# Performance work log

Hardware: AMD Instinct MI355X
Metric: run time of the kernel (lower is better)

## Reference

```python
import jax, jax.numpy as jnp
import numpy as np

B, S, H = 4, 2048, 1024
E = 8
INTER = 2816  # round(4.0*1024*2/3)=2731 -> next multiple of 256


def setup_inputs() -> dict:
    key = jax.random.key(0)
    k1, k2, k3, k4 = jax.random.split(key, 4)
    x = jax.random.normal(k1, (B, S, H), dtype=jnp.float32)
    gate_w = jax.random.normal(k2, (E, H), dtype=jnp.float32) * 0.02
    w_gate_up = jax.random.normal(k3, (E, H, 2 * INTER), dtype=jnp.float32) * 0.02
    w_down = jax.random.normal(k4, (E, INTER, H), dtype=jnp.float32) * 0.02
    return {"x": x, "gate_w": gate_w, "w_gate_up": w_gate_up, "w_down": w_down, "top_k": 2}


def _moe(x, gate_w, w_gate_up, w_down, top_k):
    Bx, Sx, Hx = x.shape
    Ex = gate_w.shape[0]
    T = Bx * Sx
    # Router
    logits = jnp.einsum('bsh,eh->bse', x, gate_w)
    probs = jax.nn.softmax(logits.astype(jnp.float32), axis=-1)  # [B,S,E] fp32
    topk_vals, topk_idx = jax.lax.top_k(probs, top_k)             # [B,S,K]
    topk_w = topk_vals / jnp.clip(topk_vals.sum(-1, keepdims=True), 1e-8)
    importance = probs.mean((0, 1))                               # [E]
    onehot = jax.nn.one_hot(topk_idx, Ex, dtype=probs.dtype)      # [B,S,K,E]
    sel_mask = onehot.sum(-2)                                     # [B,S,E] 0/1 (topk unique)
    load = sel_mask.sum((0, 1)) / (T * top_k)
    aux_loss = (Ex * (importance * load)).sum()
    # Dense combine weights per token/expert (scatter_add equivalent)
    W_full = (onehot * topk_w[..., None]).sum(-2)                 # [B,S,E]
    x_flat = x.reshape(T, Hx)
    W_flat = W_full.reshape(T, Ex).astype(x.dtype)
    out = jnp.zeros_like(x_flat)
    for e in range(Ex):  # fixed small expert loop
        gu = x_flat @ w_gate_up[e]                                # [T, 2I]
        g, u = jnp.split(gu, 2, axis=-1)
        y = (jax.nn.silu(g) * u) @ w_down[e]                      # [T, H]
        out = out + y * W_flat[:, e:e + 1]
    return out.reshape(Bx, Sx, Hx), aux_loss


def reference(x, gate_w, w_gate_up, w_down, top_k):
    return _moe(x, gate_w, w_gate_up, w_down, int(top_k))
```

## Files before the change

### kernel.cpp

```cpp
#include <hip/hip_runtime.h>

#define E_ 8
#define H_ 1024
#define I_ 2816
#define GU_ 5632
#define T_ 8192
#define NBR_ 2048

typedef __attribute__((ext_vector_type(8))) __bf16 bf16x8;
typedef __attribute__((ext_vector_type(4))) float f32x4;
typedef __attribute__((ext_vector_type(8))) unsigned short u16x8;
typedef __attribute__((ext_vector_type(4))) unsigned short u16x4;
typedef unsigned short u16;

__device__ __forceinline__ float bf2f(u16 u) {
  union { unsigned int i; float f; } v; v.i = ((unsigned int)u) << 16; return v.f;
}
__device__ __forceinline__ u16 f2bf(float f) {
  union { float f; unsigned int i; } v; v.f = f;
  unsigned int r = v.i + 0x7fffu + ((v.i >> 16) & 1u);
  return (u16)(r >> 16);
}
__device__ __forceinline__ void gld16(const void* g, void* l) {
  __builtin_amdgcn_global_load_lds((const __attribute__((address_space(1))) void*)g,
                                   (__attribute__((address_space(3))) void*)l, 16, 0, 0);
}

#define BAR() __builtin_amdgcn_s_barrier()
#define VMC(n) asm volatile("s_waitcnt vmcnt(" #n ")" ::: "memory")

__global__ __launch_bounds__(256) void k_router(
    const float* __restrict__ x, const float* __restrict__ gw,
    float* __restrict__ part_imp, int* __restrict__ part_cnt,
    int* __restrict__ tok_e, float* __restrict__ tok_w,
    u16* __restrict__ xb)
{
  __shared__ float s_imp[8];
  __shared__ int s_cnt[8];
  if (threadIdx.x < 8) { s_imp[threadIdx.x] = 0.f; s_cnt[threadIdx.x] = 0; }
  __syncthreads();

  const int t = blockIdx.x * 4 + (threadIdx.x >> 6);
  const int lane = threadIdx.x & 63;
  const float* xr = x + (size_t)t * H_;
  const f32x4* xp = (const f32x4*)(xr + lane * 16);
  f32x4 v0 = xp[0], v1 = xp[1], v2 = xp[2], v3 = xp[3];
  float xv[16];
#pragma unroll
  for (int b = 0; b < 4; ++b) { xv[b] = v0[b]; xv[4+b] = v1[b]; xv[8+b] = v2[b]; xv[12+b] = v3[b]; }
  u16x8 o0, o1;
#pragma unroll
  for (int j = 0; j < 8; ++j) { o0[j] = f2bf(xv[j]); o1[j] = f2bf(xv[8 + j]); }
  *(u16x8*)(xb + (size_t)t * H_ + lane * 16) = o0;
  *(u16x8*)(xb + (size_t)t * H_ + lane * 16 + 8) = o1;

  float lg[8];
#pragma unroll
  for (int e = 0; e < 8; ++e) {
    const f32x4* gp = (const f32x4*)(gw + e * H_ + lane * 16);
    float s = 0.f;
#pragma unroll
    for (int a = 0; a < 4; ++a) {
      f32x4 g4 = gp[a];
#pragma unroll
      for (int b = 0; b < 4; ++b) s += xv[a * 4 + b] * g4[b];
    }
    lg[e] = s;
  }
#pragma unroll
  for (int e = 0; e < 8; ++e)
#pragma unroll
    for (int off = 32; off; off >>= 1) lg[e] += __shfl_xor(lg[e], off);

  float m = lg[0];
#pragma unroll
  for (int e = 1; e < 8; ++e) m = fmaxf(m, lg[e]);
  float p[8], sum = 0.f;
#pragma unroll
  for (int e = 0; e < 8; ++e) { p[e] = __expf(lg[e] - m); sum += p[e]; }
  float inv = 1.f / sum;
#pragma unroll
  for (int e = 0; e < 8; ++e) p[e] *= inv;
  int e0 = 0;
#pragma unroll
  for (int e = 1; e < 8; ++e) if (p[e] > p[e0]) e0 = e;
  int e1 = (e0 == 0) ? 1 : 0;
#pragma unroll
  for (int e = 0; e < 8; ++e) if (e != e0 && p[e] > p[e1]) e1 = e;
  float d = 1.f / (p[e0] + p[e1]);
  if (lane == 0) {
#pragma unroll
    for (int e = 0; e < 8; ++e) atomicAdd(&s_imp[e], p[e]);
    atomicAdd(&s_cnt[e0], 1);
    atomicAdd(&s_cnt[e1], 1);
    tok_e[2 * t] = e0; tok_e[2 * t + 1] = e1;
    tok_w[2 * t] = p[e0] * d; tok_w[2 * t + 1] = p[e1] * d;
  }
  __syncthreads();
  if (threadIdx.x < 8) {
    part_imp[blockIdx.x * 8 + threadIdx.x] = s_imp[threadIdx.x];
    part_cnt[blockIdx.x * 8 + threadIdx.x] = s_cnt[threadIdx.x];
  }
}

__global__ __launch_bounds__(512) void k_reduce_scan(
    const float* __restrict__ part_imp, const int* __restrict__ part_cnt,
    int* __restrict__ counts, int* __restrict__ offsets, float* __restrict__ out)
{
  const int w = threadIdx.x >> 6, lane = threadIdx.x & 63;
  float si = 0.f; int sc = 0;
  for (int b = lane; b < NBR_; b += 64) { si += part_imp[b * 8 + w]; sc += part_cnt[b * 8 + w]; }
#pragma unroll
  for (int off = 32; off; off >>= 1) { si += __shfl_xor(si, off); sc += __shfl_xor(sc, off); }
  __shared__ float fimp[8];
  __shared__ int fcnt[8];
  if (lane == 0) { fimp[w] = si; fcnt[w] = sc; }
  __syncthreads();
  if (threadIdx.x == 0) {
    int off = 0; float aux = 0.f;
#pragma unroll
    for (int e = 0; e < 8; ++e) {
      counts[e] = fcnt[e]; offsets[e] = off; off += fcnt[e];
      aux += fimp[e] * (float)fcnt[e];
    }
    out[(size_t)T_ * H_] = 8.f * aux / ((float)T_ * (float)(2 * T_));
  }
}

__global__ __launch_bounds__(256) void k_scatter(
    const int* __restrict__ tok_e, const float* __restrict__ tok_w,
    const int* __restrict__ offsets, int* __restrict__ cursors,
    int* __restrict__ rows, float* __restrict__ wslot, int* __restrict__ t2s)
{
  __shared__ int lcnt[8], lbase[8];
  if (threadIdx.x < 8) lcnt[threadIdx.x] = 0;
  __syncthreads();
  const int t = blockIdx.x * 256 + threadIdx.x;
  const int e0 = tok_e[2 * t], e1 = tok_e[2 * t + 1];
  const int p0 = atomicAdd(&lcnt[e0], 1);
  const int p1 = atomicAdd(&lcnt[e1], 1);
  __syncthreads();
  if (threadIdx.x < 8) lbase[threadIdx.x] = atomicAdd(&cursors[threadIdx.x], lcnt[threadIdx.x]);
  __syncthreads();
  const int s0 = offsets[e0] + lbase[e0] + p0;
  const int s1 = offsets[e1] + lbase[e1] + p1;
  rows[s0] = t; wslot[s0] = tok_w[2 * t];     t2s[2 * t] = s0;
  rows[s1] = t; wslot[s1] = tok_w[2 * t + 1]; t2s[2 * t + 1] = s1;
}

__global__ __launch_bounds__(256) void k_transpose(
    const float* __restrict__ src, u16* __restrict__ dst, int R, int C)
{
  __shared__ float tile[64][68];
  const int z = blockIdx.z;
  const int c0 = blockIdx.x * 64, r0 = blockIdx.y * 64;
  const float* s = src + (size_t)z * R * C;
  u16* d = dst + (size_t)z * R * C;
  const int tx = threadIdx.x & 15, ty = threadIdx.x >> 4;
#pragma unroll
  for (int i = 0; i < 4; ++i) {
    f32x4 v = *(const f32x4*)(s + (size_t)(r0 + ty + i * 16) * C + c0 + tx * 4);
    *(f32x4*)(&tile[ty + i * 16][tx * 4]) = v;
  }
  __syncthreads();
  const int c = threadIdx.x >> 2, rq = threadIdx.x & 3;
#pragma unroll
  for (int j = 0; j < 4; ++j) {
    u16x4 w;
#pragma unroll
    for (int m = 0; m < 4; ++m) w[m] = f2bf(tile[rq * 16 + j * 4 + m][c]);
    *(u16x4*)(&d[(size_t)(c0 + c) * R + r0 + rq * 16 + j * 4]) = w;
  }
}

__global__ __launch_bounds__(256, 2) void k_gemm1(
    const u16* __restrict__ xb, const u16* __restrict__ wgu_t,
    const int* __restrict__ counts, const int* __restrict__ offsets,
    const int* __restrict__ rows, const float* __restrict__ wslot,
    u16* __restrict__ act)
{
  extern __shared__ char sh[];
  const int bid = blockIdx.x;
  const int l = (bid & 7) * 2816 + (bid >> 3);
  const int e = l / 2816;
  const int rm = l - e * 2816;
  const int xt = rm & 63, yt = rm >> 6;
  const int cnt = counts[e];
  const int m0 = xt * 128;
  if (m0 >= cnt) return;
  const int seg = offsets[e];
  const int segLast = seg + cnt - 1;
  const int n0 = yt * 64;

  const int tid = threadIdx.x;
  const int wid = tid >> 6, lane = tid & 63, l15 = lane & 15;
  const int srow = tid >> 3;
  const int scol = (((tid & 7) ^ (srow & 7)) * 8);

  const u16* wge = wgu_t + (size_t)e * GU_ * H_;

  const u16* aPtr[4];
#pragma unroll
  for (int i = 0; i < 4; ++i) {
    int slot = seg + m0 + i * 32 + srow;
    aPtr[i] = xb + (size_t)rows[slot > segLast ? segLast : slot] * H_ + scol;
  }
  const u16* bPtr[4];
  bPtr[0] = wge + (size_t)(n0 + srow) * H_ + scol;
  bPtr[1] = wge + (size_t)(n0 + 32 + srow) * H_ + scol;
  bPtr[2] = wge + (size_t)(I_ + n0 + srow) * H_ + scol;
  bPtr[3] = wge + (size_t)(I_ + n0 + 32 + srow) * H_ + scol;

  const int wm = (wid >> 1) * 64;
  const int wn = (wid & 1) * 32;

  f32x4 accg[4][2], accu[4][2];
#pragma unroll
  for (int i = 0; i < 4; ++i)
#pragma unroll
    for (int j = 0; j < 2; ++j) { accg[i][j] = (f32x4){0.f,0.f,0.f,0.f}; accu[i][j] = (f32x4){0.f,0.f,0.f,0.f}; }

#define G1_A(b, kt) { const int k0 = (kt) * 64; char* d = sh + (b) * 32768 + tid * 16;          \
    gld16(aPtr[0] + k0, d); gld16(aPtr[1] + k0, d + 4096);                                      \
    gld16(aPtr[2] + k0, d + 8192); gld16(aPtr[3] + k0, d + 12288); }
#define G1_B(b, kt) { const int k0 = (kt) * 64; char* d = sh + (b) * 32768 + 16384 + tid * 16;  \
    gld16(bPtr[0] + k0, d); gld16(bPtr[1] + k0, d + 4096);                                      \
    gld16(bPtr[2] + k0, d + 8192); gld16(bPtr[3] + k0, d + 12288); }

  const int NT = H_ / 64;
  G1_A(0, 0) G1_B(0, 0) G1_A(1, 1)
  VMC(4);
  BAR();

  int cur = 0;
  for (int t = 0; t < NT; ++t) {
    G1_B(cur ^ 1, (t + 1 < NT) ? t + 1 : NT - 1);
    const u16* As = (const u16*)(sh + cur * 32768);
    const u16* Bs = As + 8192;
#pragma unroll
    for (int ks = 0; ks < 2; ++ks) {
      const int koff = (ks * 32 + (lane >> 4) * 8) ^ ((lane & 7) * 8);
      bf16x8 a[4], bg[2], bu[2];
#pragma unroll
      for (int mf = 0; mf < 4; ++mf)
        a[mf] = *(const bf16x8*)(As + (wm + mf * 16 + l15) * 64 + koff);
#pragma unroll
      for (int nf = 0; nf < 2; ++nf) {
        bg[nf] = *(const bf16x8*)(Bs + (wn + nf * 16 + l15) * 64 + koff);
        bu[nf] = *(const bf16x8*)(Bs + (64 + wn + nf * 16 + l15) * 64 + koff);
      }
      __builtin_amdgcn_s_setprio(1);
#pragma unroll
      for (int mf = 0; mf < 4; ++mf)
#pragma unroll
        for (int nf = 0; nf < 2; ++nf) {
          accg[mf][nf] = __builtin_amdgcn_mfma_f32_16x16x32_bf16(a[mf], bg[nf], accg[mf][nf], 0, 0, 0);
          accu[mf][nf] = __builtin_amdgcn_mfma_f32_16x16x32_bf16(a[mf], bu[nf], accu[mf][nf], 0, 0, 0);
        }
      __builtin_amdgcn_s_setprio(0);
    }
    asm volatile("" ::: "memory");
    BAR();
    G1_A(cur, (t + 2 < NT) ? t + 2 : NT - 1);
    VMC(4);
    BAR();
    cur ^= 1;
  }
  VMC(0);
#undef G1_A
#undef G1_B

#pragma unroll
  for (int mf = 0; mf < 4; ++mf)
#pragma unroll
    for (int reg = 0; reg < 4; ++reg) {
      const int r = wm + mf * 16 + (lane >> 4) * 4 + reg;
      if (m0 + r >= cnt) continue;
      const int slot = seg + m0 + r;
      const float w = wslot[slot];
#pragma unroll
      for (int nf = 0; nf < 2; ++nf) {
        float g = accg[mf][nf][reg];
        float u = accu[mf][nf][reg];
        float sv = (g / (1.f + __expf(-g))) * u * w;
        act[(size_t)slot * I_ + n0 + wn + nf * 16 + l15] = f2bf(sv);
      }
    }
}

__global__ __launch_bounds__(256, 2) void k_gemm2(
    const u16* __restrict__ act, const u16* __restrict__ wd_t,
    const int* __restrict__ counts, const int* __restrict__ offsets,
    u16* __restrict__ y)
{
  extern __shared__ char sh[];
  const int bid = blockIdx.x;
  const int l = (bid & 7) * 512 + (bid >> 3);
  const int e = l >> 9;
  const int rm = l & 511;
  const int xt = rm & 63, yt = rm >> 6;
  const int cnt = counts[e];
  const int m0 = xt * 128;
  if (m0 >= cnt) return;
  const int seg = offsets[e];
  const int segLast = seg + cnt - 1;
  const int n0 = yt * 128;

  const int tid = threadIdx.x;
  const int wid = tid >> 6, lane = tid & 63, l15 = lane & 15;
  const int srow = tid >> 3;
  const int scol = (((tid & 7) ^ (srow & 7)) * 8);

  const u16* wde = wd_t + (size_t)e * H_ * I_;

  const u16* aPtr[4];
#pragma unroll
  for (int i = 0; i < 4; ++i) {
    int slot = seg + m0 + i * 32 + srow;
    aPtr[i] = act + (size_t)(slot > segLast ? segLast : slot) * I_ + scol;
  }
  const u16* bPtr[4];
#pragma unroll
  for (int i = 0; i < 4; ++i)
    bPtr[i] = wde + (size_t)(n0 + i * 32 + srow) * I_ + scol;

  const int wm = (wid >> 1) * 64;
  const int wn = (wid & 1) * 64;

  f32x4 acc[4][4];
#pragma unroll
  for (int i = 0; i < 4; ++i)
#pragma unroll
    for (int j = 0; j < 4; ++j) acc[i][j] = (f32x4){0.f,0.f,0.f,0.f};

#define G2_A(b, kt) { const int k0 = (kt) * 64; char* d = sh + (b) * 32768 + tid * 16;          \
    gld16(aPtr[0] + k0, d); gld16(aPtr[1] + k0, d + 4096);                                      \
    gld16(aPtr[2] + k0, d + 8192); gld16(aPtr[3] + k0, d + 12288); }
#define G2_B(b, kt) { const int k0 = (kt) * 64; char* d = sh + (b) * 32768 + 16384 + tid * 16;  \
    gld16(bPtr[0] + k0, d); gld16(bPtr[1] + k0, d + 4096);                                      \
    gld16(bPtr[2] + k0, d + 8192); gld16(bPtr[3] + k0, d + 12288); }

  const int NT = I_ / 64;
  G2_A(0, 0) G2_B(0, 0) G2_A(1, 1)
  VMC(4);
  BAR();

  int cur = 0;
  for (int t = 0; t < NT; ++t) {
    G2_B(cur ^ 1, (t + 1 < NT) ? t + 1 : NT - 1);
    const u16* As = (const u16*)(sh + cur * 32768);
    const u16* Bs = As + 8192;
#pragma unroll
    for (int ks = 0; ks < 2; ++ks) {
      const int koff = (ks * 32 + (lane >> 4) * 8) ^ ((lane & 7) * 8);
      bf16x8 a[4], b[4];
#pragma unroll
      for (int mf = 0; mf < 4; ++mf)
        a[mf] = *(const bf16x8*)(As + (wm + mf * 16 + l15) * 64 + koff);
#pragma unroll
      for (int nf = 0; nf < 4; ++nf)
        b[nf] = *(const bf16x8*)(Bs + (wn + nf * 16 + l15) * 64 + koff);
      __builtin_amdgcn_s_setprio(1);
#pragma unroll
      for (int mf = 0; mf < 4; ++mf)
#pragma unroll
        for (int nf = 0; nf < 4; ++nf)
          acc[mf][nf] = __builtin_amdgcn_mfma_f32_16x16x32_bf16(a[mf], b[nf], acc[mf][nf], 0, 0, 0);
      __builtin_amdgcn_s_setprio(0);
    }
    asm volatile("" ::: "memory");
    BAR();
    G2_A(cur, (t + 2 < NT) ? t + 2 : NT - 1);
    VMC(4);
    BAR();
    cur ^= 1;
  }
  VMC(0);
#undef G2_A
#undef G2_B

#pragma unroll
  for (int mf = 0; mf < 4; ++mf)
#pragma unroll
    for (int reg = 0; reg < 4; ++reg) {
      const int r = wm + mf * 16 + (lane >> 4) * 4 + reg;
      if (m0 + r >= cnt) continue;
      const int slot = seg + m0 + r;
#pragma unroll
      for (int nf = 0; nf < 4; ++nf)
        y[(size_t)slot * H_ + n0 + wn + nf * 16 + l15] = f2bf(acc[mf][nf][reg]);
    }
}

__global__ __launch_bounds__(256) void k_combine(
    const u16* __restrict__ y, const int* __restrict__ t2s, float* __restrict__ out)
{
  const size_t idx = ((size_t)blockIdx.x * 256 + threadIdx.x) * 8;
  const int t = (int)(idx >> 10);
  const int h = (int)(idx & 1023);
  const int s0 = t2s[2 * t], s1 = t2s[2 * t + 1];
  u16x8 a = *(const u16x8*)(y + (size_t)s0 * H_ + h);
  u16x8 b = *(const u16x8*)(y + (size_t)s1 * H_ + h);
  f32x4 o0, o1;
#pragma unroll
  for (int j = 0; j < 4; ++j) o0[j] = bf2f(a[j]) + bf2f(b[j]);
#pragma unroll
  for (int j = 0; j < 4; ++j) o1[j] = bf2f(a[4 + j]) + bf2f(b[4 + j]);
  *(f32x4*)(out + idx) = o0;
  *(f32x4*)(out + idx + 4) = o1;
}

extern "C" void kernel_launch(void* const* d_in, const int* in_sizes, int n_in,
                              void* d_out, int out_size, void* d_ws, size_t ws_size,
                              hipStream_t stream)
{
  const float* x   = (const float*)d_in[0];
  const float* gw  = (const float*)d_in[1];
  const float* wgu = (const float*)d_in[2];
  const float* wd  = (const float*)d_in[3];
  float* out = (float*)d_out;
  char* ws = (char*)d_ws;

  const size_t off_wgu_t = 0;
  const size_t off_wd_t  = off_wgu_t + (size_t)E_ * GU_ * H_ * 2;
  const size_t off_xb    = off_wd_t  + (size_t)E_ * H_ * I_ * 2;
  const size_t off_act   = off_xb    + (size_t)T_ * H_ * 2;
  const size_t off_ctrl  = off_act   + (size_t)2 * T_ * I_ * 2;
  const size_t need = off_ctrl + 128 + 5 * 65536;
  if (ws_size < need) return;

  u16* wgu_t = (u16*)(ws + off_wgu_t);
  u16* wd_t  = (u16*)(ws + off_wd_t);
  u16* xb    = (u16*)(ws + off_xb);
  u16* act   = (u16*)(ws + off_act);
  u16* y     = (u16*)(ws + off_wgu_t);
  float* part_imp = (float*)(ws + off_act);
  int*   part_cnt = (int*)(ws + off_act + (size_t)NBR_ * 8 * 4);
  char* ctrl = ws + off_ctrl;
  int*   counts  = (int*)(ctrl + 0);
  int*   cursors = (int*)(ctrl + 32);
  int*   offsets = (int*)(ctrl + 64);
  int*   tok_e   = (int*)(ctrl + 128);
  float* tok_w   = (float*)(ctrl + 128 + 1 * 65536);
  int*   rows    = (int*)(ctrl + 128 + 2 * 65536);
  float* wslot   = (float*)(ctrl + 128 + 3 * 65536);
  int*   t2s     = (int*)(ctrl + 128 + 4 * 65536);

  static bool attr_done = false;
  if (!attr_done) {
    hipFuncSetAttribute((const void*)k_gemm1, hipFuncAttributeMaxDynamicSharedMemorySize, 65536);
    hipFuncSetAttribute((const void*)k_gemm2, hipFuncAttributeMaxDynamicSharedMemorySize, 65536);
    attr_done = true;
  }

  hipMemsetAsync(ctrl, 0, 96, stream);
  hipLaunchKernelGGL(k_transpose, dim3(GU_ / 64, H_ / 64, E_), dim3(256), 0, stream, wgu, wgu_t, H_, GU_);
  hipLaunchKernelGGL(k_transpose, dim3(H_ / 64, I_ / 64, E_), dim3(256), 0, stream, wd, wd_t, I_, H_);
  hipLaunchKernelGGL(k_router, dim3(NBR_), dim3(256), 0, stream, x, gw, part_imp, part_cnt, tok_e, tok_w, xb);
  hipLaunchKernelGGL(k_reduce_scan, dim3(1), dim3(512), 0, stream, part_imp, part_cnt, counts, offsets, out);
  hipLaunchKernelGGL(k_scatter, dim3(T_ / 256), dim3(256), 0, stream, tok_e, tok_w, offsets, cursors, rows, wslot, t2s);
  hipLaunchKernelGGL(k_gemm1, dim3((I_ / 64) * 64 * E_), dim3(256), 65536, stream, xb, wgu_t, counts, offsets, rows, wslot, act);
  hipLaunchKernelGGL(k_gemm2, dim3((H_ / 128) * 64 * E_), dim3(256), 65536, stream, act, wd_t, counts, offsets, y);
  hipLaunchKernelGGL(k_combine, dim3((T_ * H_) / (256 * 8)), dim3(256), 0, stream, y, t2s, out);
}
```

Before: 545.8 us.

## Replace double-buffered LDS pipeline with single-buffer loop and higher occupancy

Both grouped GEMM kernels drop the two-stage double-buffered global-to-LDS prefetch and use a single 32KB static LDS buffer, loading each K tile and then synchronizing before compute. Launch bounds rise from 2 to 4 blocks per CU, relying on occupancy instead of software pipelining to hide memory latency. The dynamic shared-memory attribute setup is removed. This halves LDS per block but exposes load latency within each block and adds a full barrier wait on every iteration.

```diff
diff --git a/kernel.cpp b/kernel.cpp
--- a/kernel.cpp
+++ b/kernel.cpp
@@ -26,9 +26,6 @@
                                    (__attribute__((address_space(3))) void*)l, 16, 0, 0);
 }
 
-#define BAR() __builtin_amdgcn_s_barrier()
-#define VMC(n) asm volatile("s_waitcnt vmcnt(" #n ")" ::: "memory")
-
 __global__ __launch_bounds__(256) void k_router(
     const float* __restrict__ x, const float* __restrict__ gw,
     float* __restrict__ part_imp, int* __restrict__ part_cnt,
@@ -173,13 +170,13 @@
   }
 }
 
-__global__ __launch_bounds__(256, 2) void k_gemm1(
+__global__ __launch_bounds__(256, 4) void k_gemm1(
     const u16* __restrict__ xb, const u16* __restrict__ wgu_t,
     const int* __restrict__ counts, const int* __restrict__ offsets,
     const int* __restrict__ rows, const float* __restrict__ wslot,
     u16* __restrict__ act)
 {
-  extern __shared__ char sh[];
+  __shared__ alignas(16) char sh[32768];
   const int bid = blockIdx.x;
   const int l = (bid & 7) * 2816 + (bid >> 3);
   const int e = l / 2816;
@@ -220,22 +217,20 @@
 #pragma unroll
     for (int j = 0; j < 2; ++j) { accg[i][j] = (f32x4){0.f,0.f,0.f,0.f}; accu[i][j] = (f32x4){0.f,0.f,0.f,0.f}; }
 
-#define G1_A(b, kt) { const int k0 = (kt) * 64; char* d = sh + (b) * 32768 + tid * 16;          \
-    gld16(aPtr[0] + k0, d); gld16(aPtr[1] + k0, d + 4096);                                      \
-    gld16(aPtr[2] + k0, d + 8192); gld16(aPtr[3] + k0, d + 12288); }
-#define G1_B(b, kt) { const int k0 = (kt) * 64; char* d = sh + (b) * 32768 + 16384 + tid * 16;  \
-    gld16(bPtr[0] + k0, d); gld16(bPtr[1] + k0, d + 4096);                                      \
-    gld16(bPtr[2] + k0, d + 8192); gld16(bPtr[3] + k0, d + 12288); }
-
   const int NT = H_ / 64;
-  G1_A(0, 0) G1_B(0, 0) G1_A(1, 1)
-  VMC(4);
-  BAR();
-
-  int cur = 0;
   for (int t = 0; t < NT; ++t) {
-    G1_B(cur ^ 1, (t + 1 < NT) ? t + 1 : NT - 1);
-    const u16* As = (const u16*)(sh + cur * 32768);
+    {
+      char* dA = sh + tid * 16;
+      gld16(aPtr[0], dA); gld16(aPtr[1], dA + 4096);
+      gld16(aPtr[2], dA + 8192); gld16(aPtr[3], dA + 12288);
+      char* dB = sh + 16384 + tid * 16;
+      gld16(bPtr[0], dB); gld16(bPtr[1], dB + 4096);
+      gld16(bPtr[2], dB + 8192); gld16(bPtr[3], dB + 12288);
+#pragma unroll
+      for (int i = 0; i < 4; ++i) { aPtr[i] += 64; bPtr[i] += 64; }
+    }
+    __syncthreads();
+    const u16* As = (const u16*)sh;
     const u16* Bs = As + 8192;
 #pragma unroll
     for (int ks = 0; ks < 2; ++ks) {
@@ -259,16 +254,8 @@
         }
       __builtin_amdgcn_s_setprio(0);
     }
-    asm volatile("" ::: "memory");
-    BAR();
-    G1_A(cur, (t + 2 < NT) ? t + 2 : NT - 1);
-    VMC(4);
-    BAR();
-    cur ^= 1;
-  }
-  VMC(0);
-#undef G1_A
-#undef G1_B
+    __syncthreads();
+  }
 
 #pragma unroll
   for (int mf = 0; mf < 4; ++mf)
@@ -288,12 +275,12 @@
     }
 }
 
-__global__ __launch_bounds__(256, 2) void k_gemm2(
+__global__ __launch_bounds__(256, 4) void k_gemm2(
     const u16* __restrict__ act, const u16* __restrict__ wd_t,
     const int* __restrict__ counts, const int* __restrict__ offsets,
     u16* __restrict__ y)
 {
-  extern __shared__ char sh[];
+  __shared__ alignas(16) char sh[32768];
   const int bid = blockIdx.x;
   const int l = (bid & 7) * 512 + (bid >> 3);
   const int e = l >> 9;
@@ -333,22 +320,20 @@
 #pragma unroll
     for (int j = 0; j < 4; ++j) acc[i][j] = (f32x4){0.f,0.f,0.f,0.f};
 
-#define G2_A(b, kt) { const int k0 = (kt) * 64; char* d = sh + (b) * 32768 + tid * 16;          \
-    gld16(aPtr[0] + k0, d); gld16(aPtr[1] + k0, d + 4096);                                      \
-    gld16(aPtr[2] + k0, d + 8192); gld16(aPtr[3] + k0, d + 12288); }
-#define G2_B(b, kt) { const int k0 = (kt) * 64; char* d = sh + (b) * 32768 + 16384 + tid * 16;  \
-    gld16(bPtr[0] + k0, d); gld16(bPtr[1] + k0, d + 4096);                                      \
-    gld16(bPtr[2] + k0, d + 8192); gld16(bPtr[3] + k0, d + 12288); }
-
   const int NT = I_ / 64;
-  G2_A(0, 0) G2_B(0, 0) G2_A(1, 1)
-  VMC(4);
-  BAR();
-
-  int cur = 0;
   for (int t = 0; t < NT; ++t) {
-    G2_B(cur ^ 1, (t + 1 < NT) ? t + 1 : NT - 1);
-    const u16* As = (const u16*)(sh + cur * 32768);
+    {
+      char* dA = sh + tid * 16;
+      gld16(aPtr[0], dA); gld16(aPtr[1], dA + 4096);
+      gld16(aPtr[2], dA + 8192); gld16(aPtr[3], dA + 12288);
+      char* dB = sh + 16384 + tid * 16;
+      gld16(bPtr[0], dB); gld16(bPtr[1], dB + 4096);
+      gld16(bPtr[2], dB + 8192); gld16(bPtr[3], dB + 12288);
+#pragma unroll
+      for (int i = 0; i < 4; ++i) { aPtr[i] += 64; bPtr[i] += 64; }
+    }
+    __syncthreads();
+    const u16* As = (const u16*)sh;
     const u16* Bs = As + 8192;
 #pragma unroll
     for (int ks = 0; ks < 2; ++ks) {
@@ -368,16 +353,8 @@
           acc[mf][nf] = __builtin_amdgcn_mfma_f32_16x16x32_bf16(a[mf], b[nf], acc[mf][nf], 0, 0, 0);
       __builtin_amdgcn_s_setprio(0);
     }
-    asm volatile("" ::: "memory");
-    BAR();
-    G2_A(cur, (t + 2 < NT) ? t + 2 : NT - 1);
-    VMC(4);
-    BAR();
-    cur ^= 1;
-  }
-  VMC(0);
-#undef G2_A
-#undef G2_B
+    __syncthreads();
+  }
 
 #pragma unroll
   for (int mf = 0; mf < 4; ++mf)
@@ -446,20 +423,13 @@
   float* wslot   = (float*)(ctrl + 128 + 3 * 65536);
   int*   t2s     = (int*)(ctrl + 128 + 4 * 65536);
 
-  static bool attr_done = false;
-  if (!attr_done) {
-    hipFuncSetAttribute((const void*)k_gemm1, hipFuncAttributeMaxDynamicSharedMemorySize, 65536);
-    hipFuncSetAttribute((const void*)k_gemm2, hipFuncAttributeMaxDynamicSharedMemorySize, 65536);
-    attr_done = true;
-  }
-
   hipMemsetAsync(ctrl, 0, 96, stream);
   hipLaunchKernelGGL(k_transpose, dim3(GU_ / 64, H_ / 64, E_), dim3(256), 0, stream, wgu, wgu_t, H_, GU_);
   hipLaunchKernelGGL(k_transpose, dim3(H_ / 64, I_ / 64, E_), dim3(256), 0, stream, wd, wd_t, I_, H_);
   hipLaunchKernelGGL(k_router, dim3(NBR_), dim3(256), 0, stream, x, gw, part_imp, part_cnt, tok_e, tok_w, xb);
   hipLaunchKernelGGL(k_reduce_scan, dim3(1), dim3(512), 0, stream, part_imp, part_cnt, counts, offsets, out);
   hipLaunchKernelGGL(k_scatter, dim3(T_ / 256), dim3(256), 0, stream, tok_e, tok_w, offsets, cursors, rows, wslot, t2s);
-  hipLaunchKernelGGL(k_gemm1, dim3((I_ / 64) * 64 * E_), dim3(256), 65536, stream, xb, wgu_t, counts, offsets, rows, wslot, act);
-  hipLaunchKernelGGL(k_gemm2, dim3((H_ / 128) * 64 * E_), dim3(256), 65536, stream, act, wd_t, counts, offsets, y);
+  hipLaunchKernelGGL(k_gemm1, dim3((I_ / 64) * 64 * E_), dim3(256), 0, stream, xb, wgu_t, counts, offsets, rows, wslot, act);
+  hipLaunchKernelGGL(k_gemm2, dim3((H_ / 128) * 64 * E_), dim3(256), 0, stream, act, wd_t, counts, offsets, y);
   hipLaunchKernelGGL(k_combine, dim3((T_ * H_) / (256 * 8)), dim3(256), 0, stream, y, t2s, out);
 }
```

After: 548.5 us. About the same (+0.5%).

## Enlarge expert GEMM tiles to 256-row, 8-wave blocks with interleaved ping-pong schedule

Applied to the files above, without the earlier changes.

Both grouped expert GEMMs move from 128-row tiles with 4 waves to 256-row by 128-column tiles with 8 waves (512 threads) and 128 KB of double-buffered LDS. Each K-step is split into four quarter-phases in which LDS reads, async global-to-LDS loads of the next tiles and MFMA bursts are interleaved under explicit barriers, lgkmcnt waits and scheduling barriers. The aim is to raise arithmetic intensity per loaded byte and overlap memory traffic with matrix math. In exchange, LDS use caps residency at one block per CU, accumulator register pressure doubles, and the extra barriers may cost more than they save.

```diff
diff --git a/kernel.cpp b/kernel.cpp
--- a/kernel.cpp
+++ b/kernel.cpp
@@ -27,6 +27,8 @@
 }
 
 #define BAR() __builtin_amdgcn_s_barrier()
+#define SB0() __builtin_amdgcn_sched_barrier(0)
+#define LGKM0() asm volatile("s_waitcnt lgkmcnt(0)" ::: "memory")
 #define VMC(n) asm volatile("s_waitcnt vmcnt(" #n ")" ::: "memory")
 
 __global__ __launch_bounds__(256) void k_router(
@@ -173,7 +175,7 @@
   }
 }
 
-__global__ __launch_bounds__(256, 2) void k_gemm1(
+__global__ __launch_bounds__(512, 2) void k_gemm1(
     const u16* __restrict__ xb, const u16* __restrict__ wgu_t,
     const int* __restrict__ counts, const int* __restrict__ offsets,
     const int* __restrict__ rows, const float* __restrict__ wslot,
@@ -181,126 +183,12 @@
 {
   extern __shared__ char sh[];
   const int bid = blockIdx.x;
-  const int l = (bid & 7) * 2816 + (bid >> 3);
-  const int e = l / 2816;
-  const int rm = l - e * 2816;
+  const int l = (bid & 7) * 1408 + (bid >> 3);
+  const int e = l / 1408;
+  const int rm = l - e * 1408;
   const int xt = rm & 63, yt = rm >> 6;
   const int cnt = counts[e];
-  const int m0 = xt * 128;
-  if (m0 >= cnt) return;
-  const int seg = offsets[e];
-  const int segLast = seg + cnt - 1;
-  const int n0 = yt * 64;
-
-  const int tid = threadIdx.x;
-  const int wid = tid >> 6, lane = tid & 63, l15 = lane & 15;
-  const int srow = tid >> 3;
-  const int scol = (((tid & 7) ^ (srow & 7)) * 8);
-
-  const u16* wge = wgu_t + (size_t)e * GU_ * H_;
-
-  const u16* aPtr[4];
-#pragma unroll
-  for (int i = 0; i < 4; ++i) {
-    int slot = seg + m0 + i * 32 + srow;
-    aPtr[i] = xb + (size_t)rows[slot > segLast ? segLast : slot] * H_ + scol;
-  }
-  const u16* bPtr[4];
-  bPtr[0] = wge + (size_t)(n0 + srow) * H_ + scol;
-  bPtr[1] = wge + (size_t)(n0 + 32 + srow) * H_ + scol;
-  bPtr[2] = wge + (size_t)(I_ + n0 + srow) * H_ + scol;
-  bPtr[3] = wge + (size_t)(I_ + n0 + 32 + srow) * H_ + scol;
-
-  const int wm = (wid >> 1) * 64;
-  const int wn = (wid & 1) * 32;
-
-  f32x4 accg[4][2], accu[4][2];
-#pragma unroll
-  for (int i = 0; i < 4; ++i)
-#pragma unroll
-    for (int j = 0; j < 2; ++j) { accg[i][j] = (f32x4){0.f,0.f,0.f,0.f}; accu[i][j] = (f32x4){0.f,0.f,0.f,0.f}; }
-
-#define G1_A(b, kt) { const int k0 = (kt) * 64; char* d = sh + (b) * 32768 + tid * 16;          \
-    gld16(aPtr[0] + k0, d); gld16(aPtr[1] + k0, d + 4096);                                      \
-    gld16(aPtr[2] + k0, d + 8192); gld16(aPtr[3] + k0, d + 12288); }
-#define G1_B(b, kt) { const int k0 = (kt) * 64; char* d = sh + (b) * 32768 + 16384 + tid * 16;  \
-    gld16(bPtr[0] + k0, d); gld16(bPtr[1] + k0, d + 4096);                                      \
-    gld16(bPtr[2] + k0, d + 8192); gld16(bPtr[3] + k0, d + 12288); }
-
-  const int NT = H_ / 64;
-  G1_A(0, 0) G1_B(0, 0) G1_A(1, 1)
-  VMC(4);
-  BAR();
-
-  int cur = 0;
-  for (int t = 0; t < NT; ++t) {
-    G1_B(cur ^ 1, (t + 1 < NT) ? t + 1 : NT - 1);
-    const u16* As = (const u16*)(sh + cur * 32768);
-    const u16* Bs = As + 8192;
-#pragma unroll
-    for (int ks = 0; ks < 2; ++ks) {
-      const int koff = (ks * 32 + (lane >> 4) * 8) ^ ((lane & 7) * 8);
-      bf16x8 a[4], bg[2], bu[2];
-#pragma unroll
-      for (int mf = 0; mf < 4; ++mf)
-        a[mf] = *(const bf16x8*)(As + (wm + mf * 16 + l15) * 64 + koff);
-#pragma unroll
-      for (int nf = 0; nf < 2; ++nf) {
-        bg[nf] = *(const bf16x8*)(Bs + (wn + nf * 16 + l15) * 64 + koff);
-        bu[nf] = *(const bf16x8*)(Bs + (64 + wn + nf * 16 + l15) * 64 + koff);
-      }
-      __builtin_amdgcn_s_setprio(1);
-#pragma unroll
-      for (int mf = 0; mf < 4; ++mf)
-#pragma unroll
-        for (int nf = 0; nf < 2; ++nf) {
-          accg[mf][nf] = __builtin_amdgcn_mfma_f32_16x16x32_bf16(a[mf], bg[nf], accg[mf][nf], 0, 0, 0);
-          accu[mf][nf] = __builtin_amdgcn_mfma_f32_16x16x32_bf16(a[mf], bu[nf], accu[mf][nf], 0, 0, 0);
-        }
-      __builtin_amdgcn_s_setprio(0);
-    }
-    asm volatile("" ::: "memory");
-    BAR();
-    G1_A(cur, (t + 2 < NT) ? t + 2 : NT - 1);
-    VMC(4);
-    BAR();
-    cur ^= 1;
-  }
-  VMC(0);
-#undef G1_A
-#undef G1_B
-
-#pragma unroll
-  for (int mf = 0; mf < 4; ++mf)
-#pragma unroll
-    for (int reg = 0; reg < 4; ++reg) {
-      const int r = wm + mf * 16 + (lane >> 4) * 4 + reg;
-      if (m0 + r >= cnt) continue;
-      const int slot = seg + m0 + r;
-      const float w = wslot[slot];
-#pragma unroll
-      for (int nf = 0; nf < 2; ++nf) {
-        float g = accg[mf][nf][reg];
-        float u = accu[mf][nf][reg];
-        float sv = (g / (1.f + __expf(-g))) * u * w;
-        act[(size_t)slot * I_ + n0 + wn + nf * 16 + l15] = f2bf(sv);
-      }
-    }
-}
-
-__global__ __launch_bounds__(256, 2) void k_gemm2(
-    const u16* __restrict__ act, const u16* __restrict__ wd_t,
-    const int* __restrict__ counts, const int* __restrict__ offsets,
-    u16* __restrict__ y)
-{
-  extern __shared__ char sh[];
-  const int bid = blockIdx.x;
-  const int l = (bid & 7) * 512 + (bid >> 3);
-  const int e = l >> 9;
-  const int rm = l & 511;
-  const int xt = rm & 63, yt = rm >> 6;
-  const int cnt = counts[e];
-  const int m0 = xt * 128;
+  const int m0 = xt * 256;
   if (m0 >= cnt) return;
   const int seg = offsets[e];
   const int segLast = seg + cnt - 1;
@@ -308,87 +196,234 @@
 
   const int tid = threadIdx.x;
   const int wid = tid >> 6, lane = tid & 63, l15 = lane & 15;
+  const int wr = wid >> 2, wc = wid & 3;
   const int srow = tid >> 3;
   const int scol = (((tid & 7) ^ (srow & 7)) * 8);
 
-  const u16* wde = wd_t + (size_t)e * H_ * I_;
-
-  const u16* aPtr[4];
-#pragma unroll
-  for (int i = 0; i < 4; ++i) {
-    int slot = seg + m0 + i * 32 + srow;
-    aPtr[i] = act + (size_t)(slot > segLast ? segLast : slot) * I_ + scol;
-  }
-  const u16* bPtr[4];
-#pragma unroll
-  for (int i = 0; i < 4; ++i)
-    bPtr[i] = wde + (size_t)(n0 + i * 32 + srow) * I_ + scol;
-
-  const int wm = (wid >> 1) * 64;
-  const int wn = (wid & 1) * 64;
-
-  f32x4 acc[4][4];
-#pragma unroll
-  for (int i = 0; i < 4; ++i)
-#pragma unroll
-    for (int j = 0; j < 4; ++j) acc[i][j] = (f32x4){0.f,0.f,0.f,0.f};
-
-#define G2_A(b, kt) { const int k0 = (kt) * 64; char* d = sh + (b) * 32768 + tid * 16;          \
-    gld16(aPtr[0] + k0, d); gld16(aPtr[1] + k0, d + 4096);                                      \
-    gld16(aPtr[2] + k0, d + 8192); gld16(aPtr[3] + k0, d + 12288); }
-#define G2_B(b, kt) { const int k0 = (kt) * 64; char* d = sh + (b) * 32768 + 16384 + tid * 16;  \
-    gld16(bPtr[0] + k0, d); gld16(bPtr[1] + k0, d + 4096);                                      \
-    gld16(bPtr[2] + k0, d + 8192); gld16(bPtr[3] + k0, d + 12288); }
-
-  const int NT = I_ / 64;
-  G2_A(0, 0) G2_B(0, 0) G2_A(1, 1)
-  VMC(4);
-  BAR();
+  const u16* wge = wgu_t + (size_t)e * GU_ * H_;
+
+  const u16* aP[4];
+#pragma unroll
+  for (int g = 0; g < 4; ++g) {
+    int slot = seg + m0 + g * 64 + srow;
+    aP[g] = xb + (size_t)rows[slot > segLast ? segLast : slot] * H_ + scol;
+  }
+  const u16* bP[4];
+#pragma unroll
+  for (int j = 0; j < 4; ++j) {
+    int i = j & 1, half = j >> 1;
+    int br = (i * 2 + (srow >> 5)) * 64 + half * 32 + (srow & 31);
+    int g16 = br >> 4, sub = br & 15;
+    int grow = ((g16 & 1) ? I_ : 0) + n0 + (g16 >> 1) * 16 + sub;
+    bP[j] = wge + (size_t)grow * H_ + scol;
+  }
+
+  int koffs[2];
+#pragma unroll
+  for (int ks = 0; ks < 2; ++ks)
+    koffs[ks] = ((ks * 32 + (lane >> 4) * 8) ^ ((lane & 7) * 8)) * 2;
+
+  f32x4 accg[8][2], accu[8][2];
+#pragma unroll
+  for (int i = 0; i < 8; ++i)
+#pragma unroll
+    for (int j = 0; j < 2; ++j) { accg[i][j] = (f32x4){0.f,0.f,0.f,0.f}; accu[i][j] = (f32x4){0.f,0.f,0.f,0.f}; }
+
+#define ST_Aa(b, kt) { char* d = sh + (b)*65536 + tid*16;          gld16(aP[0]+(kt)*64, d); gld16(aP[2]+(kt)*64, d+8192); }
+#define ST_Ab(b, kt) { char* d = sh + (b)*65536 + 16384 + tid*16;  gld16(aP[1]+(kt)*64, d); gld16(aP[3]+(kt)*64, d+8192); }
+#define ST_Ba(b, kt) { char* d = sh + (b)*65536 + 32768 + tid*16;  gld16(bP[0]+(kt)*64, d); gld16(bP[1]+(kt)*64, d+8192); }
+#define ST_Bb(b, kt) { char* d = sh + (b)*65536 + 49152 + tid*16;  gld16(bP[2]+(kt)*64, d); gld16(bP[3]+(kt)*64, d+8192); }
+#define RD_A(MH) _Pragma("unroll") for (int ks=0;ks<2;++ks) _Pragma("unroll") for (int mf=0;mf<4;++mf) \
+  af[ks][mf] = *(const bf16x8*)(bufp + (MH)*16384 + (wr*64 + mf*16 + l15)*128 + koffs[ks]);
+#define RD_B(NH, DST) _Pragma("unroll") for (int ks=0;ks<2;++ks) _Pragma("unroll") for (int nfp=0;nfp<2;++nfp) \
+  DST[ks][nfp] = *(const bf16x8*)(bufp + 32768 + (NH)*16384 + (wc*32 + nfp*16 + l15)*128 + koffs[ks]);
+#define MM_G1(MB, CG, BSRC) \
+  __builtin_amdgcn_s_setprio(1); \
+  _Pragma("unroll") for (int ks=0;ks<2;++ks) _Pragma("unroll") for (int mf=0;mf<4;++mf) { \
+    accg[(MB)+mf][CG] = __builtin_amdgcn_mfma_f32_16x16x32_bf16(af[ks][mf], BSRC[ks][0], accg[(MB)+mf][CG],0,0,0); \
+    accu[(MB)+mf][CG] = __builtin_amdgcn_mfma_f32_16x16x32_bf16(af[ks][mf], BSRC[ks][1], accu[(MB)+mf][CG],0,0,0); \
+  } \
+  __builtin_amdgcn_s_setprio(0);
+
+  const int NT = H_ / 64;
+  ST_Aa(0,0) ST_Ba(0,0) ST_Ab(0,0) ST_Bb(0,0)
+  ST_Aa(1,1) ST_Ba(1,1) ST_Ab(1,1)
+  VMC(6); BAR();
 
   int cur = 0;
   for (int t = 0; t < NT; ++t) {
-    G2_B(cur ^ 1, (t + 1 < NT) ? t + 1 : NT - 1);
-    const u16* As = (const u16*)(sh + cur * 32768);
-    const u16* Bs = As + 8192;
-#pragma unroll
-    for (int ks = 0; ks < 2; ++ks) {
-      const int koff = (ks * 32 + (lane >> 4) * 8) ^ ((lane & 7) * 8);
-      bf16x8 a[4], b[4];
-#pragma unroll
-      for (int mf = 0; mf < 4; ++mf)
-        a[mf] = *(const bf16x8*)(As + (wm + mf * 16 + l15) * 64 + koff);
-#pragma unroll
-      for (int nf = 0; nf < 4; ++nf)
-        b[nf] = *(const bf16x8*)(Bs + (wn + nf * 16 + l15) * 64 + koff);
-      __builtin_amdgcn_s_setprio(1);
-#pragma unroll
-      for (int mf = 0; mf < 4; ++mf)
-#pragma unroll
-        for (int nf = 0; nf < 4; ++nf)
-          acc[mf][nf] = __builtin_amdgcn_mfma_f32_16x16x32_bf16(a[mf], b[nf], acc[mf][nf], 0, 0, 0);
-      __builtin_amdgcn_s_setprio(0);
-    }
-    asm volatile("" ::: "memory");
-    BAR();
-    G2_A(cur, (t + 2 < NT) ? t + 2 : NT - 1);
-    VMC(4);
+    const int nx1 = (t + 1 < NT) ? t + 1 : NT - 1;
+    const int nx2 = (t + 2 < NT) ? t + 2 : NT - 1;
+    const char* bufp = sh + cur * 65536;
+    bf16x8 af[2][4], bLo[2][2], bHi[2][2];
+    RD_A(0) RD_B(0, bLo)
+    ST_Bb(cur ^ 1, nx1)
+    BAR(); LGKM0(); SB0();
+    MM_G1(0, 0, bLo)
+    BAR();
+    RD_B(1, bHi)
+    ST_Aa(cur, nx2)
+    BAR(); LGKM0(); SB0();
+    MM_G1(0, 1, bHi)
+    BAR();
+    RD_A(1)
+    ST_Ba(cur, nx2)
+    BAR(); LGKM0(); SB0();
+    MM_G1(4, 0, bLo)
+    BAR();
+    ST_Ab(cur, nx2)
+    BAR();
+    MM_G1(4, 1, bHi)
+    VMC(6);
     BAR();
     cur ^= 1;
   }
   VMC(0);
-#undef G2_A
-#undef G2_B
-
-#pragma unroll
-  for (int mf = 0; mf < 4; ++mf)
+#undef ST_Aa
+#undef ST_Ab
+#undef ST_Ba
+#undef ST_Bb
+#undef RD_A
+#undef RD_B
+#undef MM_G1
+
+#pragma unroll
+  for (int mf = 0; mf < 8; ++mf)
 #pragma unroll
     for (int reg = 0; reg < 4; ++reg) {
-      const int r = wm + mf * 16 + (lane >> 4) * 4 + reg;
+      const int r = wr * 128 + mf * 16 + (lane >> 4) * 4 + reg;
       if (m0 + r >= cnt) continue;
       const int slot = seg + m0 + r;
+      const float w = wslot[slot];
+#pragma unroll
+      for (int cg = 0; cg < 2; ++cg) {
+        float g = accg[mf][cg][reg];
+        float u = accu[mf][cg][reg];
+        float sv = (g / (1.f + __expf(-g))) * u * w;
+        act[(size_t)slot * I_ + n0 + wc * 32 + cg * 16 + l15] = f2bf(sv);
+      }
+    }
+}
+
+__global__ __launch_bounds__(512, 2) void k_gemm2(
+    const u16* __restrict__ act, const u16* __restrict__ wd_t,
+    const int* __restrict__ counts, const int* __restrict__ offsets,
+    u16* __restrict__ y)
+{
+  extern __shared__ char sh[];
+  const int bid = blockIdx.x;
+  const int l = (bid & 7) * 256 + (bid >> 3);
+  const int e = l >> 8;
+  const int rm = l & 255;
+  const int xt = rm & 63, yt = rm >> 6;
+  const int cnt = counts[e];
+  const int m0 = xt * 256;
+  if (m0 >= cnt) return;
+  const int seg = offsets[e];
+  const int segLast = seg + cnt - 1;
+  const int n0 = yt * 256;
+
+  const int tid = threadIdx.x;
+  const int wid = tid >> 6, lane = tid & 63, l15 = lane & 15;
+  const int wr = wid >> 2, wc = wid & 3;
+  const int srow = tid >> 3;
+  const int scol = (((tid & 7) ^ (srow & 7)) * 8);
+
+  const u16* wde = wd_t + (size_t)e * H_ * I_;
+
+  const u16* aP[4];
+#pragma unroll
+  for (int g = 0; g < 4; ++g) {
+    int slot = seg + m0 + g * 64 + srow;
+    aP[g] = act + (size_t)(slot > segLast ? segLast : slot) * I_ + scol;
+  }
+  const u16* bP[4];
+#pragma unroll
+  for (int j = 0; j < 4; ++j) {
+    int i = j & 1, half = j >> 1;
+    int br = (i * 2 + (srow >> 5)) * 64 + half * 32 + (srow & 31);
+    bP[j] = wde + (size_t)(n0 + br) * I_ + scol;
+  }
+
+  int koffs[2];
+#pragma unroll
+  for (int ks = 0; ks < 2; ++ks)
+    koffs[ks] = ((ks * 32 + (lane >> 4) * 8) ^ ((lane & 7) * 8)) * 2;
+
+  f32x4 acc[8][4];
+#pragma unroll
+  for (int i = 0; i < 8; ++i)
+#pragma unroll
+    for (int j = 0; j < 4; ++j) acc[i][j] = (f32x4){0.f,0.f,0.f,0.f};
+
+#define ST_Aa(b, kt) { char* d = sh + (b)*65536 + tid*16;          gld16(aP[0]+(kt)*64, d); gld16(aP[2]+(kt)*64, d+8192); }
+#define ST_Ab(b, kt) { char* d = sh + (b)*65536 + 16384 + tid*16;  gld16(aP[1]+(kt)*64, d); gld16(aP[3]+(kt)*64, d+8192); }
+#define ST_Ba(b, kt) { char* d = sh + (b)*65536 + 32768 + tid*16;  gld16(bP[0]+(kt)*64, d); gld16(bP[1]+(kt)*64, d+8192); }
+#define ST_Bb(b, kt) { char* d = sh + (b)*65536 + 49152 + tid*16;  gld16(bP[2]+(kt)*64, d); gld16(bP[3]+(kt)*64, d+8192); }
+#define RD_A(MH) _Pragma("unroll") for (int ks=0;ks<2;++ks) _Pragma("unroll") for (int mf=0;mf<4;++mf) \
+  af[ks][mf] = *(const bf16x8*)(bufp + (MH)*16384 + (wr*64 + mf*16 + l15)*128 + koffs[ks]);
+#define RD_B(NH, DST) _Pragma("unroll") for (int ks=0;ks<2;++ks) _Pragma("unroll") for (int nfp=0;nfp<2;++nfp) \
+  DST[ks][nfp] = *(const bf16x8*)(bufp + 32768 + (NH)*16384 + (wc*32 + nfp*16 + l15)*128 + koffs[ks]);
+#define MM_G2(MB, NH, BSRC) \
+  __builtin_amdgcn_s_setprio(1); \
+  _Pragma("unroll") for (int ks=0;ks<2;++ks) _Pragma("unroll") for (int mf=0;mf<4;++mf) { \
+    acc[(MB)+mf][(NH)*2+0] = __builtin_amdgcn_mfma_f32_16x16x32_bf16(af[ks][mf], BSRC[ks][0], acc[(MB)+mf][(NH)*2+0],0,0,0); \
+    acc[(MB)+mf][(NH)*2+1] = __builtin_amdgcn_mfma_f32_16x16x32_bf16(af[ks][mf], BSRC[ks][1], acc[(MB)+mf][(NH)*2+1],0,0,0); \
+  } \
+  __builtin_amdgcn_s_setprio(0);
+
+  const int NT = I_ / 64;
+  ST_Aa(0,0) ST_Ba(0,0) ST_Ab(0,0) ST_Bb(0,0)
+  ST_Aa(1,1) ST_Ba(1,1) ST_Ab(1,1)
+  VMC(6); BAR();
+
+  int cur = 0;
+  for (int t = 0; t < NT; ++t) {
+    const int nx1 = (t + 1 < NT) ? t + 1 : NT - 1;
+    const int nx2 = (t + 2 < NT) ? t + 2 : NT - 1;
+    const char* bufp = sh + cur * 65536;
+    bf16x8 af[2][4], bLo[2][2], bHi[2][2];
+    RD_A(0) RD_B(0, bLo)
+    ST_Bb(cur ^ 1, nx1)
+    BAR(); LGKM0(); SB0();
+    MM_G2(0, 0, bLo)
+    BAR();
+    RD_B(1, bHi)
+    ST_Aa(cur, nx2)
+    BAR(); LGKM0(); SB0();
+    MM_G2(0, 1, bHi)
+    BAR();
+    RD_A(1)
+    ST_Ba(cur, nx2)
+    BAR(); LGKM0(); SB0();
+    MM_G2(4, 0, bLo)
+    BAR();
+    ST_Ab(cur, nx2)
+    BAR();
+    MM_G2(4, 1, bHi)
+    VMC(6);
+    BAR();
+    cur ^= 1;
+  }
+  VMC(0);
+#undef ST_Aa
+#undef ST_Ab
+#undef ST_Ba
+#undef ST_Bb
+#undef RD_A
+#undef RD_B
+#undef MM_G2
+
+#pragma unroll
+  for (int mf = 0; mf < 8; ++mf)
+#pragma unroll
+    for (int reg = 0; reg < 4; ++reg) {
+      const int r = wr * 128 + mf * 16 + (lane >> 4) * 4 + reg;
+      if (m0 + r >= cnt) continue;
+      const int slot = seg + m0 + r;
 #pragma unroll
       for (int nf = 0; nf < 4; ++nf)
-        y[(size_t)slot * H_ + n0 + wn + nf * 16 + l15] = f2bf(acc[mf][nf][reg]);
+        y[(size_t)slot * H_ + n0 + wc * 64 + nf * 16 + l15] = f2bf(acc[mf][nf][reg]);
     }
 }
 
@@ -448,8 +483,8 @@
 
   static bool attr_done = false;
   if (!attr_done) {
-    hipFuncSetAttribute((const void*)k_gemm1, hipFuncAttributeMaxDynamicSharedMemorySize, 65536);
-    hipFuncSetAttribute((const void*)k_gemm2, hipFuncAttributeMaxDynamicSharedMemorySize, 65536);
+    hipFuncSetAttribute((const void*)k_gemm1, hipFuncAttributeMaxDynamicSharedMemorySize, 131072);
+    hipFuncSetAttribute((const void*)k_gemm2, hipFuncAttributeMaxDynamicSharedMemorySize, 131072);
     attr_done = true;
   }
 
@@ -459,7 +494,7 @@
   hipLaunchKernelGGL(k_router, dim3(NBR_), dim3(256), 0, stream, x, gw, part_imp, part_cnt, tok_e, tok_w, xb);
   hipLaunchKernelGGL(k_reduce_scan, dim3(1), dim3(512), 0, stream, part_imp, part_cnt, counts, offsets, out);
   hipLaunchKernelGGL(k_scatter, dim3(T_ / 256), dim3(256), 0, stream, tok_e, tok_w, offsets, cursors, rows, wslot, t2s);
-  hipLaunchKernelGGL(k_gemm1, dim3((I_ / 64) * 64 * E_), dim3(256), 65536, stream, xb, wgu_t, counts, offsets, rows, wslot, act);
-  hipLaunchKernelGGL(k_gemm2, dim3((H_ / 128) * 64 * E_), dim3(256), 65536, stream, act, wd_t, counts, offsets, y);
+  hipLaunchKernelGGL(k_gemm1, dim3(8 * 1408), dim3(512), 131072, stream, xb, wgu_t, counts, offsets, rows, wslot, act);
+  hipLaunchKernelGGL(k_gemm2, dim3(8 * 256), dim3(512), 131072, stream, act, wd_t, counts, offsets, y);
   hipLaunchKernelGGL(k_combine, dim3((T_ * H_) / (256 * 8)), dim3(256), 0, stream, y, t2s, out);
 }
```

After: 562.4 us. 3.0% more time.
